# Optimization experiments

Hardware: AMD Instinct MI355X
Metric: run time of the kernel (lower is better)

The kernel has to match this reference:

```python
import jax, jax.numpy as jnp
import numpy as np

N_USERS = 100_000
N_ENTITIES = 400_000
N_NODES = N_USERS + N_ENTITIES  # 500k
DIM = 64
N_EDGES = 2_000_000
BATCH = 4096
N_LAYERS = 3
CF_WEIGHT = 1.0
L2_REG = 1e-4


def setup_inputs() -> dict:
    key = jax.random.key(0)
    k_emb, k_e, k_u, k_p, k_n = jax.random.split(key, 5)
    # xavier_uniform on (N, D): bound = sqrt(6/(N+D))
    bound = float(np.sqrt(6.0 / (N_NODES + DIM)))
    emb = jax.random.uniform(k_emb, (N_NODES, DIM), jnp.float32, -bound, bound)
    edge_index = jax.random.randint(k_e, (2, N_EDGES), 0, N_NODES, dtype=jnp.int32)
    user_idx = jax.random.randint(k_u, (BATCH,), 0, N_USERS, dtype=jnp.int32)
    pos_item = jax.random.randint(k_p, (BATCH,), 0, N_NODES, dtype=jnp.int32)
    neg_item = jax.random.randint(k_n, (BATCH,), 0, N_NODES, dtype=jnp.int32)
    return {"emb": emb, "edge_index": edge_index, "user_idx": user_idx,
            "pos_item": pos_item, "neg_item": neg_item}


def _lightgcn(emb, edge_index, n_layers):
    # LGConv(normalize=True): x' = D^{-1/2} A D^{-1/2} x, no self loops.
    n = emb.shape[0]
    src, dst = edge_index[0], edge_index[1]
    deg = jax.ops.segment_sum(jnp.ones_like(dst, dtype=emb.dtype), dst,
                              num_segments=n)
    dinv = jnp.where(deg > 0, jax.lax.rsqrt(jnp.maximum(deg, 1e-12)), 0.0)
    norm = dinv[src] * dinv[dst]  # [E]
    x = emb
    acc = emb  # layer-0 term of the mean over stacked layers
    for _ in range(n_layers):
        msgs = x[src] * norm[:, None]  # [E, D] gather + scale
        x = jax.ops.segment_sum(msgs, dst, num_segments=n)  # scatter-add
        acc = acc + x
    return acc / (n_layers + 1)  # mean over (layers+1) stacked embeddings


def reference(emb, edge_index, user_idx, pos_item, neg_item):
    all_layer = _lightgcn(emb, edge_index, N_LAYERS)
    u = all_layer[user_idx]
    p = all_layer[pos_item]
    n_ = all_layer[neg_item]
    pos_score = jnp.sum(u * p, axis=-1)
    neg_score = jnp.sum(u * n_, axis=-1)
    # BPRLoss: -mean(logsigmoid(pos - neg)) == mean(softplus(neg - pos))
    cf_loss = jnp.mean(jax.nn.softplus(neg_score - pos_score))
    u_ego = emb[user_idx]
    p_ego = emb[pos_item]
    n_ego = emb[neg_item]
    reg_loss = 0.5 * (jnp.sum(u_ego ** 2) + jnp.sum(p_ego ** 2)
                      + jnp.sum(n_ego ** 2)) / float(BATCH)
    return CF_WEIGHT * cf_loss + L2_REG * reg_loss
```

## Files before the change

kernel.cpp:

```cpp
#include <hip/hip_runtime.h>
#include <cstdint>
#include <cstddef>

#define N_USERS   100000
#define N_NODES   500000
#define DIM       64
#define N_EDGES   2000000
#define BATCH     4096
#define SCAN_B    1024
#define NBLK      ((N_NODES + SCAN_B - 1) / SCAN_B)
#define X1C_CAP   350000
#define LA_CAP    150000

typedef unsigned char uchar;
typedef unsigned short ushort;
typedef unsigned int uint;

__device__ __forceinline__ ushort f2bf(float f) {
    uint u = __float_as_uint(f);
    uint r = u + 0x7FFFu + ((u >> 16) & 1u);
    return (ushort)(r >> 16);
}
__device__ __forceinline__ float bflo(uint u) { return __uint_as_float(u << 16); }
__device__ __forceinline__ float bfhi(uint u) { return __uint_as_float(u & 0xFFFF0000u); }

__global__ void k_degexp(const int* __restrict__ src, const int* __restrict__ dst,
                         int* __restrict__ deg, const uchar* __restrict__ f3,
                         uchar* __restrict__ fA) {
    int t = blockIdx.x * blockDim.x + threadIdx.x;
    if (t < N_EDGES / 4) {
        int4 s = ((const int4*)src)[t];
        int4 d = ((const int4*)dst)[t];
        atomicAdd(&deg[d.x], 1); atomicAdd(&deg[d.y], 1);
        atomicAdd(&deg[d.z], 1); atomicAdd(&deg[d.w], 1);
        if (f3[d.x] && !fA[s.x]) fA[s.x] = 1;
        if (f3[d.y] && !fA[s.y]) fA[s.y] = 1;
        if (f3[d.z] && !fA[s.z]) fA[s.z] = 1;
        if (f3[d.w] && !fA[s.w]) fA[s.w] = 1;
    }
}

__global__ void k_expand(const int* __restrict__ src, const int* __restrict__ dst,
                         const uchar* __restrict__ fin, uchar* __restrict__ fout) {
    int t = blockIdx.x * blockDim.x + threadIdx.x;
    if (t < N_EDGES / 4) {
        int4 s = ((const int4*)src)[t];
        int4 d = ((const int4*)dst)[t];
        if (fin[d.x] && !fout[s.x]) fout[s.x] = 1;
        if (fin[d.y] && !fout[s.y]) fout[s.y] = 1;
        if (fin[d.z] && !fout[s.z]) fout[s.z] = 1;
        if (fin[d.w] && !fout[s.w]) fout[s.w] = 1;
    }
}

__global__ void k_mark(const int* __restrict__ u, const int* __restrict__ p,
                       const int* __restrict__ n, uchar* __restrict__ f3,
                       uchar* __restrict__ fA, uchar* __restrict__ fB) {
    int i = blockIdx.x * blockDim.x + threadIdx.x;
    if (i >= 3 * BATCH) return;
    int idx;
    if (i < BATCH)          idx = u[i];
    else if (i < 2 * BATCH) idx = p[i - BATCH];
    else                    idx = n[i - 2 * BATCH];
    f3[idx] = 1; fA[idx] = 1; fB[idx] = 1;
}

__global__ void k_scanA(const int* __restrict__ deg, const uchar* __restrict__ fA,
                        const uchar* __restrict__ fB, int* __restrict__ bsumD,
                        int* __restrict__ bsumP) {
    __shared__ int sD[SCAN_B];
    __shared__ int sP[SCAN_B];
    int i = blockIdx.x * SCAN_B + threadIdx.x;
    int d = 0, pk = 0;
    if (i < N_NODES) { d = deg[i]; pk = (int)fA[i] | ((int)fB[i] << 16); }
    sD[threadIdx.x] = d; sP[threadIdx.x] = pk;
    __syncthreads();
    for (int off = SCAN_B / 2; off; off >>= 1) {
        if (threadIdx.x < off) {
            sD[threadIdx.x] += sD[threadIdx.x + off];
            sP[threadIdx.x] += sP[threadIdx.x + off];
        }
        __syncthreads();
    }
    if (threadIdx.x == 0) { bsumD[blockIdx.x] = sD[0]; bsumP[blockIdx.x] = sP[0]; }
}

__global__ void k_scanB(const int* __restrict__ bsumD, const int* __restrict__ bsumP,
                        int* __restrict__ boffD, int* __restrict__ boffA,
                        int* __restrict__ boffB, int* __restrict__ counts,
                        int* __restrict__ rowstart_tail) {
    __shared__ int sD[512];
    __shared__ int sA[512];
    __shared__ int sB[512];
    int d = (threadIdx.x < NBLK) ? bsumD[threadIdx.x] : 0;
    int p = (threadIdx.x < NBLK) ? bsumP[threadIdx.x] : 0;
    int a = p & 0xFFFF, b = p >> 16;
    sD[threadIdx.x] = d; sA[threadIdx.x] = a; sB[threadIdx.x] = b;
    __syncthreads();
    for (int off = 1; off < 512; off <<= 1) {
        int tD = (threadIdx.x >= off) ? sD[threadIdx.x - off] : 0;
        int tA = (threadIdx.x >= off) ? sA[threadIdx.x - off] : 0;
        int tB = (threadIdx.x >= off) ? sB[threadIdx.x - off] : 0;
        __syncthreads();
        sD[threadIdx.x] += tD; sA[threadIdx.x] += tA; sB[threadIdx.x] += tB;
        __syncthreads();
    }
    if (threadIdx.x < NBLK) {
        boffD[threadIdx.x] = sD[threadIdx.x] - d;
        boffA[threadIdx.x] = sA[threadIdx.x] - a;
        boffB[threadIdx.x] = sB[threadIdx.x] - b;
    }
    if (threadIdx.x == 511) {
        counts[0] = sA[511]; counts[1] = sB[511];
        rowstart_tail[0] = N_EDGES;
    }
}

__global__ void k_scanC(const int* __restrict__ deg, const uchar* __restrict__ fA,
                        const uchar* __restrict__ fB,
                        const int* __restrict__ boffD, const int* __restrict__ boffA,
                        const int* __restrict__ boffB,
                        int* __restrict__ rowstart, int* __restrict__ cursor,
                        float* __restrict__ dinv, int* __restrict__ mapA,
                        int* __restrict__ mapB, int4* __restrict__ listA4,
                        int4* __restrict__ listB4) {
    __shared__ int sD[SCAN_B];
    __shared__ int sP[SCAN_B];
    int i = blockIdx.x * SCAN_B + threadIdx.x;
    int d = 0, a = 0, b = 0;
    if (i < N_NODES) { d = deg[i]; a = (int)fA[i]; b = (int)fB[i]; }
    sD[threadIdx.x] = d; sP[threadIdx.x] = a | (b << 16);
    __syncthreads();
    for (int off = 1; off < SCAN_B; off <<= 1) {
        int tD = (threadIdx.x >= off) ? sD[threadIdx.x - off] : 0;
        int tP = (threadIdx.x >= off) ? sP[threadIdx.x - off] : 0;
        __syncthreads();
        sD[threadIdx.x] += tD; sP[threadIdx.x] += tP;
        __syncthreads();
    }
    if (i < N_NODES) {
        int exD = sD[threadIdx.x] - d + boffD[blockIdx.x];
        int incP = sP[threadIdx.x];
        int exA = (incP & 0xFFFF) - a + boffA[blockIdx.x];
        int exB = (incP >> 16) - b + boffB[blockIdx.x];
        rowstart[i] = exD;
        cursor[i] = exD;
        float dv = (d > 0) ? rsqrtf((float)d) : 0.0f;
        dinv[i] = dv;
        mapA[i] = a ? exA : -1;
        mapB[i] = b ? exB : -1;
        int4 ent = make_int4(exD, exD + d, __float_as_int(dv), 0);
        if (a) listA4[exA] = ent;
        if (b) listB4[exB] = ent;
    }
}

__global__ void k_conv(const float* __restrict__ emb, const float* __restrict__ dinv,
                       ushort* __restrict__ embs) {
    int c = blockIdx.x * blockDim.x + threadIdx.x;
    if (c < N_NODES * 16) {
        int row = c >> 4;
        float4 v = ((const float4*)emb)[c];
        float dv = dinv[row];
        uint2 o;
        o.x = (uint)f2bf(v.x * dv) | ((uint)f2bf(v.y * dv) << 16);
        o.y = (uint)f2bf(v.z * dv) | ((uint)f2bf(v.w * dv) << 16);
        ((uint2*)embs)[c] = o;
    }
}

__global__ void k_scatter(const int* __restrict__ src, const int* __restrict__ dst,
                          const uchar* __restrict__ fB,
                          int* __restrict__ cursor, int* __restrict__ csr_src) {
    int t = blockIdx.x * blockDim.x + threadIdx.x;
    if (t < N_EDGES / 4) {
        int4 s = ((const int4*)src)[t];
        int4 d = ((const int4*)dst)[t];
        if (fB[d.x]) csr_src[atomicAdd(&cursor[d.x], 1)] = s.x;
        if (fB[d.y]) csr_src[atomicAdd(&cursor[d.y], 1)] = s.y;
        if (fB[d.z]) csr_src[atomicAdd(&cursor[d.z], 1)] = s.z;
        if (fB[d.w]) csr_src[atomicAdd(&cursor[d.w], 1)] = s.w;
    }
}

__global__ void k_prop1(const ushort* __restrict__ embs, const int4* __restrict__ listB4,
                        const int* __restrict__ counts, const int* __restrict__ csr_src,
                        ushort* __restrict__ x1c) {
    int lane = threadIdx.x & 63;
    int wv = (blockIdx.x * blockDim.x + threadIdx.x) >> 6;
    if (wv >= counts[1]) return;
    int4 nb = listB4[wv];
    int sub = lane >> 4, q = lane & 15;
    float4 acc = {0.f, 0.f, 0.f, 0.f};
    for (int i = nb.x + sub; i < nb.y; i += 4) {
        int s = csr_src[i];
        uint2 u = *(const uint2*)(embs + (size_t)s * DIM + q * 4);
        acc.x += bflo(u.x); acc.y += bfhi(u.x);
        acc.z += bflo(u.y); acc.w += bfhi(u.y);
    }
    for (int off = 16; off <= 32; off <<= 1) {
        acc.x += __shfl_xor(acc.x, off, 64);
        acc.y += __shfl_xor(acc.y, off, 64);
        acc.z += __shfl_xor(acc.z, off, 64);
        acc.w += __shfl_xor(acc.w, off, 64);
    }
    if (sub == 0) {
        float dv = __int_as_float(nb.z);
        float d2 = dv * dv;
        uint2 o;
        o.x = (uint)f2bf(acc.x * d2) | ((uint)f2bf(acc.y * d2) << 16);
        o.y = (uint)f2bf(acc.z * d2) | ((uint)f2bf(acc.w * d2) << 16);
        *(uint2*)(x1c + (size_t)wv * DIM + q * 4) = o;
    }
}

__global__ void k_prop2(const ushort* __restrict__ x1c, const int* __restrict__ mapB,
                        const int4* __restrict__ listA4, const int* __restrict__ counts,
                        const int* __restrict__ csr_src, ushort* __restrict__ x2c) {
    int lane = threadIdx.x & 63;
    int wv = (blockIdx.x * blockDim.x + threadIdx.x) >> 6;
    if (wv >= counts[0]) return;
    int4 nb = listA4[wv];
    int sub = lane >> 4, q = lane & 15;
    float4 acc = {0.f, 0.f, 0.f, 0.f};
    for (int i = nb.x + sub; i < nb.y; i += 4) {
        int s = csr_src[i];
        int slot = mapB[s];
        uint2 u = *(const uint2*)(x1c + (size_t)slot * DIM + q * 4);
        acc.x += bflo(u.x); acc.y += bfhi(u.x);
        acc.z += bflo(u.y); acc.w += bfhi(u.y);
    }
    for (int off = 16; off <= 32; off <<= 1) {
        acc.x += __shfl_xor(acc.x, off, 64);
        acc.y += __shfl_xor(acc.y, off, 64);
        acc.z += __shfl_xor(acc.z, off, 64);
        acc.w += __shfl_xor(acc.w, off, 64);
    }
    if (sub == 0) {
        float dv = __int_as_float(nb.z);
        float d2 = dv * dv;
        uint2 o;
        o.x = (uint)f2bf(acc.x * d2) | ((uint)f2bf(acc.y * d2) << 16);
        o.y = (uint)f2bf(acc.z * d2) | ((uint)f2bf(acc.w * d2) << 16);
        *(uint2*)(x2c + (size_t)wv * DIM + q * 4) = o;
    }
}

__global__ void k_prop3(const ushort* __restrict__ x2c, const int* __restrict__ mapA,
                        const int* __restrict__ u, const int* __restrict__ p,
                        const int* __restrict__ n, const float* __restrict__ dinv,
                        const int* __restrict__ rowstart, const int* __restrict__ csr_src,
                        float* __restrict__ x3c) {
    int lane = threadIdx.x & 63;
    int wv = (blockIdx.x * blockDim.x + threadIdx.x) >> 6;
    if (wv >= 3 * BATCH) return;
    int t;
    if (wv < BATCH)          t = u[wv];
    else if (wv < 2 * BATCH) t = p[wv - BATCH];
    else                     t = n[wv - 2 * BATCH];
    int sub = lane >> 4, q = lane & 15;
    int b = rowstart[t], e = rowstart[t + 1];
    float4 acc = {0.f, 0.f, 0.f, 0.f};
    for (int i = b + sub; i < e; i += 4) {
        int s = csr_src[i];
        int slot = mapA[s];
        uint2 uu = *(const uint2*)(x2c + (size_t)slot * DIM + q * 4);
        acc.x += bflo(uu.x); acc.y += bfhi(uu.x);
        acc.z += bflo(uu.y); acc.w += bfhi(uu.y);
    }
    for (int off = 16; off <= 32; off <<= 1) {
        acc.x += __shfl_xor(acc.x, off, 64);
        acc.y += __shfl_xor(acc.y, off, 64);
        acc.z += __shfl_xor(acc.z, off, 64);
        acc.w += __shfl_xor(acc.w, off, 64);
    }
    if (sub == 0) {
        float dv = dinv[t];
        float4 o = {acc.x * dv, acc.y * dv, acc.z * dv, acc.w * dv};
        ((float4*)x3c)[(size_t)wv * 16 + q] = o;
    }
}

__global__ void k_loss(const float* __restrict__ emb, const ushort* __restrict__ x1c,
                       const ushort* __restrict__ x2c, const float* __restrict__ x3c,
                       const int* __restrict__ mapA, const int* __restrict__ mapB,
                       const float* __restrict__ dinv,
                       const int* __restrict__ u, const int* __restrict__ p,
                       const int* __restrict__ n, float* __restrict__ out) {
    int lane = threadIdx.x & 63;
    int w = (blockIdx.x * blockDim.x + threadIdx.x) >> 6;
    if (w >= BATCH) return;
    int ui = u[w], pi = p[w], ni = n[w];
    float dvu = dinv[ui], dvp = dinv[pi], dvn = dinv[ni];
    float rdu = dvu > 0.f ? 1.f / dvu : 0.f;
    float rdp = dvp > 0.f ? 1.f / dvp : 0.f;
    float rdn = dvn > 0.f ? 1.f / dvn : 0.f;
    float ue = emb[(size_t)ui * DIM + lane];
    float pe = emb[(size_t)pi * DIM + lane];
    float ne = emb[(size_t)ni * DIM + lane];
    float u1 = __uint_as_float((uint)x1c[(size_t)mapB[ui] * DIM + lane] << 16) * rdu;
    float p1 = __uint_as_float((uint)x1c[(size_t)mapB[pi] * DIM + lane] << 16) * rdp;
    float n1 = __uint_as_float((uint)x1c[(size_t)mapB[ni] * DIM + lane] << 16) * rdn;
    float u2 = __uint_as_float((uint)x2c[(size_t)mapA[ui] * DIM + lane] << 16) * rdu;
    float p2 = __uint_as_float((uint)x2c[(size_t)mapA[pi] * DIM + lane] << 16) * rdp;
    float n2 = __uint_as_float((uint)x2c[(size_t)mapA[ni] * DIM + lane] << 16) * rdn;
    float uall = 0.25f * (ue + u1 + u2 + x3c[(size_t)w * DIM + lane]);
    float pall = 0.25f * (pe + p1 + p2 + x3c[(size_t)(BATCH + w) * DIM + lane]);
    float nall = 0.25f * (ne + n1 + n2 + x3c[(size_t)(2 * BATCH + w) * DIM + lane]);
    float pos = uall * pall;
    float neg = uall * nall;
    float sq  = ue * ue + pe * pe + ne * ne;
    for (int off = 32; off; off >>= 1) {
        pos += __shfl_xor(pos, off, 64);
        neg += __shfl_xor(neg, off, 64);
        sq  += __shfl_xor(sq,  off, 64);
    }
    if (lane == 0) {
        float z = neg - pos;
        float sp = fmaxf(z, 0.0f) + log1pf(expf(-fabsf(z)));
        float contrib = sp * (1.0f / BATCH) + 1e-4f * 0.5f * sq * (1.0f / BATCH);
        atomicAdd(out, contrib);
    }
}

extern "C" void kernel_launch(void* const* d_in, const int* in_sizes, int n_in,
                              void* d_out, int out_size, void* d_ws, size_t ws_size,
                              hipStream_t stream) {
    const float* emb  = (const float*)d_in[0];
    const int*   edge = (const int*)d_in[1];
    const int*   src  = edge;
    const int*   dst  = edge + N_EDGES;
    const int*   uidx = (const int*)d_in[2];
    const int*   pidx = (const int*)d_in[3];
    const int*   nidx = (const int*)d_in[4];
    float* out = (float*)d_out;

    char* w = (char*)d_ws;
    ushort* embs    = (ushort*)w;                w += (size_t)N_NODES * DIM * 2;
    ushort* x1c     = (ushort*)w;                w += (size_t)X1C_CAP * DIM * 2;
    ushort* x2c     = (ushort*)w;                w += (size_t)LA_CAP * DIM * 2;
    float*  x3c     = (float*)w;                 w += (size_t)3 * BATCH * DIM * 4;
    float*  dinv    = (float*)w;                 w += (size_t)N_NODES * 4;
    int*    deg     = (int*)w;                   w += (size_t)N_NODES * 4;
    int*    rowstart= (int*)w;                   w += (size_t)(N_NODES + 4) * 4;
    int*    cursor  = (int*)w;                   w += (size_t)N_NODES * 4;
    int*    csr_src = (int*)w;                   w += (size_t)N_EDGES * 4;
    int*    mapA    = (int*)w;                   w += (size_t)N_NODES * 4;
    int*    mapB    = (int*)w;                   w += (size_t)N_NODES * 4;
    int4*   listA4  = (int4*)w;                  w += (size_t)LA_CAP * 16;
    int4*   listB4  = (int4*)w;                  w += (size_t)X1C_CAP * 16;
    uchar*  flags   = (uchar*)w;                 w += (size_t)3 * N_NODES;
    uchar*  f3 = flags;
    uchar*  fA = flags + N_NODES;
    uchar*  fB = flags + 2 * N_NODES;
    int*    bsumD   = (int*)w;                   w += (size_t)NBLK * 4;
    int*    boffD   = (int*)w;                   w += (size_t)NBLK * 4;
    int*    bsumP   = (int*)w;                   w += (size_t)NBLK * 4;
    int*    boffA   = (int*)w;                   w += (size_t)NBLK * 4;
    int*    boffB   = (int*)w;                   w += (size_t)NBLK * 4;
    int*    counts  = (int*)w;                   w += 16;

    hipMemsetAsync(deg, 0, (size_t)N_NODES * 4, stream);
    hipMemsetAsync(flags, 0, (size_t)3 * N_NODES, stream);
    hipMemsetAsync(out, 0, 4, stream);

    k_mark<<<(3 * BATCH + 255) / 256, 256, 0, stream>>>(uidx, pidx, nidx, f3, fA, fB);
    k_degexp<<<(N_EDGES / 4 + 255) / 256, 256, 0, stream>>>(src, dst, deg, f3, fA);
    k_expand<<<(N_EDGES / 4 + 255) / 256, 256, 0, stream>>>(src, dst, fA, fB);

    k_scanA<<<NBLK, SCAN_B, 0, stream>>>(deg, fA, fB, bsumD, bsumP);
    k_scanB<<<1, 512, 0, stream>>>(bsumD, bsumP, boffD, boffA, boffB, counts,
                                   rowstart + N_NODES);
    k_scanC<<<NBLK, SCAN_B, 0, stream>>>(deg, fA, fB, boffD, boffA, boffB,
                                         rowstart, cursor, dinv, mapA, mapB,
                                         listA4, listB4);

    k_conv<<<(N_NODES * 16 + 255) / 256, 256, 0, stream>>>(emb, dinv, embs);

    k_scatter<<<(N_EDGES / 4 + 255) / 256, 256, 0, stream>>>(src, dst, fB, cursor, csr_src);

    const int PT = 256;
    k_prop1<<<((size_t)X1C_CAP * 64 + PT - 1) / PT, PT, 0, stream>>>(
        embs, listB4, counts, csr_src, x1c);
    k_prop2<<<((size_t)LA_CAP * 64 + PT - 1) / PT, PT, 0, stream>>>(
        x1c, mapB, listA4, counts, csr_src, x2c);
    k_prop3<<<(3 * BATCH * 64 + PT - 1) / PT, PT, 0, stream>>>(
        x2c, mapA, uidx, pidx, nidx, dinv, rowstart, csr_src, x3c);

    k_loss<<<(BATCH * 64 + 255) / 256, 256, 0, stream>>>(
        emb, x1c, x2c, x3c, mapA, mapB, dinv, uidx, pidx, nidx, out);
}
```

Measured before the change: 501.9 us.

## Pack node flags into bitmasks and degrees/cursors into byte-packed counters

```diff
diff --git a/kernel.cpp b/kernel.cpp
--- a/kernel.cpp
+++ b/kernel.cpp
@@ -9,6 +9,8 @@
 #define BATCH     4096
 #define SCAN_B    1024
 #define NBLK      ((N_NODES + SCAN_B - 1) / SCAN_B)
+#define NMASKW    ((N_NODES + 31) / 32)
+#define NPACK     ((N_NODES + 3) / 4)
 #define X1C_CAP   350000
 #define LA_CAP    150000
 
@@ -24,55 +26,70 @@
 __device__ __forceinline__ float bflo(uint u) { return __uint_as_float(u << 16); }
 __device__ __forceinline__ float bfhi(uint u) { return __uint_as_float(u & 0xFFFF0000u); }
 
-__global__ void k_degexp(const int* __restrict__ src, const int* __restrict__ dst,
-                         int* __restrict__ deg, const uchar* __restrict__ f3,
-                         uchar* __restrict__ fA) {
-    int t = blockIdx.x * blockDim.x + threadIdx.x;
-    if (t < N_EDGES / 4) {
-        int4 s = ((const int4*)src)[t];
-        int4 d = ((const int4*)dst)[t];
-        atomicAdd(&deg[d.x], 1); atomicAdd(&deg[d.y], 1);
-        atomicAdd(&deg[d.z], 1); atomicAdd(&deg[d.w], 1);
-        if (f3[d.x] && !fA[s.x]) fA[s.x] = 1;
-        if (f3[d.y] && !fA[s.y]) fA[s.y] = 1;
-        if (f3[d.z] && !fA[s.z]) fA[s.z] = 1;
-        if (f3[d.w] && !fA[s.w]) fA[s.w] = 1;
-    }
-}
-
-__global__ void k_expand(const int* __restrict__ src, const int* __restrict__ dst,
-                         const uchar* __restrict__ fin, uchar* __restrict__ fout) {
-    int t = blockIdx.x * blockDim.x + threadIdx.x;
-    if (t < N_EDGES / 4) {
-        int4 s = ((const int4*)src)[t];
-        int4 d = ((const int4*)dst)[t];
-        if (fin[d.x] && !fout[s.x]) fout[s.x] = 1;
-        if (fin[d.y] && !fout[s.y]) fout[s.y] = 1;
-        if (fin[d.z] && !fout[s.z]) fout[s.z] = 1;
-        if (fin[d.w] && !fout[s.w]) fout[s.w] = 1;
-    }
+__device__ __forceinline__ int getbit(const uint* __restrict__ w, int i) {
+    return (w[i >> 5] >> (i & 31)) & 1;
+}
+__device__ __forceinline__ void setbit(uint* w, int i) {
+    uint m = 1u << (i & 31);
+    if (!(w[i >> 5] & m)) atomicOr(&w[i >> 5], m);
 }
 
 __global__ void k_mark(const int* __restrict__ u, const int* __restrict__ p,
-                       const int* __restrict__ n, uchar* __restrict__ f3,
-                       uchar* __restrict__ fA, uchar* __restrict__ fB) {
+                       const int* __restrict__ n, uint* __restrict__ f3w,
+                       uint* __restrict__ fAw, uint* __restrict__ fBw) {
     int i = blockIdx.x * blockDim.x + threadIdx.x;
     if (i >= 3 * BATCH) return;
     int idx;
     if (i < BATCH)          idx = u[i];
     else if (i < 2 * BATCH) idx = p[i - BATCH];
     else                    idx = n[i - 2 * BATCH];
-    f3[idx] = 1; fA[idx] = 1; fB[idx] = 1;
-}
-
-__global__ void k_scanA(const int* __restrict__ deg, const uchar* __restrict__ fA,
-                        const uchar* __restrict__ fB, int* __restrict__ bsumD,
+    atomicOr(&f3w[idx >> 5], 1u << (idx & 31));
+    atomicOr(&fAw[idx >> 5], 1u << (idx & 31));
+    atomicOr(&fBw[idx >> 5], 1u << (idx & 31));
+}
+
+__global__ void k_degexp(const int* __restrict__ src, const int* __restrict__ dst,
+                         uint* __restrict__ degP, const uint* __restrict__ f3w,
+                         uint* __restrict__ fAw) {
+    int t = blockIdx.x * blockDim.x + threadIdx.x;
+    if (t < N_EDGES / 4) {
+        int4 s = ((const int4*)src)[t];
+        int4 d = ((const int4*)dst)[t];
+        atomicAdd(&degP[d.x >> 2], 1u << ((d.x & 3) * 8));
+        atomicAdd(&degP[d.y >> 2], 1u << ((d.y & 3) * 8));
+        atomicAdd(&degP[d.z >> 2], 1u << ((d.z & 3) * 8));
+        atomicAdd(&degP[d.w >> 2], 1u << ((d.w & 3) * 8));
+        if (getbit(f3w, d.x)) setbit(fAw, s.x);
+        if (getbit(f3w, d.y)) setbit(fAw, s.y);
+        if (getbit(f3w, d.z)) setbit(fAw, s.z);
+        if (getbit(f3w, d.w)) setbit(fAw, s.w);
+    }
+}
+
+__global__ void k_expand(const int* __restrict__ src, const int* __restrict__ dst,
+                         const uint* __restrict__ fAw, uint* __restrict__ fBw) {
+    int t = blockIdx.x * blockDim.x + threadIdx.x;
+    if (t < N_EDGES / 4) {
+        int4 s = ((const int4*)src)[t];
+        int4 d = ((const int4*)dst)[t];
+        if (getbit(fAw, d.x)) setbit(fBw, s.x);
+        if (getbit(fAw, d.y)) setbit(fBw, s.y);
+        if (getbit(fAw, d.z)) setbit(fBw, s.z);
+        if (getbit(fAw, d.w)) setbit(fBw, s.w);
+    }
+}
+
+__global__ void k_scanA(const uint* __restrict__ degP, const uint* __restrict__ fAw,
+                        const uint* __restrict__ fBw, int* __restrict__ bsumD,
                         int* __restrict__ bsumP) {
     __shared__ int sD[SCAN_B];
     __shared__ int sP[SCAN_B];
     int i = blockIdx.x * SCAN_B + threadIdx.x;
     int d = 0, pk = 0;
-    if (i < N_NODES) { d = deg[i]; pk = (int)fA[i] | ((int)fB[i] << 16); }
+    if (i < N_NODES) {
+        d = (degP[i >> 2] >> ((i & 3) * 8)) & 0xFF;
+        pk = getbit(fAw, i) | (getbit(fBw, i) << 16);
+    }
     sD[threadIdx.x] = d; sP[threadIdx.x] = pk;
     __syncthreads();
     for (int off = SCAN_B / 2; off; off >>= 1) {
@@ -116,19 +133,21 @@
     }
 }
 
-__global__ void k_scanC(const int* __restrict__ deg, const uchar* __restrict__ fA,
-                        const uchar* __restrict__ fB,
+__global__ void k_scanC(const uint* __restrict__ degP, const uint* __restrict__ fAw,
+                        const uint* __restrict__ fBw,
                         const int* __restrict__ boffD, const int* __restrict__ boffA,
                         const int* __restrict__ boffB,
-                        int* __restrict__ rowstart, int* __restrict__ cursor,
-                        float* __restrict__ dinv, int* __restrict__ mapA,
-                        int* __restrict__ mapB, int4* __restrict__ listA4,
-                        int4* __restrict__ listB4) {
+                        int* __restrict__ rowstart, float* __restrict__ dinv,
+                        int* __restrict__ mapA, int* __restrict__ mapB,
+                        int4* __restrict__ listA4, int4* __restrict__ listB4) {
     __shared__ int sD[SCAN_B];
     __shared__ int sP[SCAN_B];
     int i = blockIdx.x * SCAN_B + threadIdx.x;
     int d = 0, a = 0, b = 0;
-    if (i < N_NODES) { d = deg[i]; a = (int)fA[i]; b = (int)fB[i]; }
+    if (i < N_NODES) {
+        d = (degP[i >> 2] >> ((i & 3) * 8)) & 0xFF;
+        a = getbit(fAw, i); b = getbit(fBw, i);
+    }
     sD[threadIdx.x] = d; sP[threadIdx.x] = a | (b << 16);
     __syncthreads();
     for (int off = 1; off < SCAN_B; off <<= 1) {
@@ -144,7 +163,6 @@
         int exA = (incP & 0xFFFF) - a + boffA[blockIdx.x];
         int exB = (incP >> 16) - b + boffB[blockIdx.x];
         rowstart[i] = exD;
-        cursor[i] = exD;
         float dv = (d > 0) ? rsqrtf((float)d) : 0.0f;
         dinv[i] = dv;
         mapA[i] = a ? exA : -1;
@@ -170,16 +188,20 @@
 }
 
 __global__ void k_scatter(const int* __restrict__ src, const int* __restrict__ dst,
-                          const uchar* __restrict__ fB,
-                          int* __restrict__ cursor, int* __restrict__ csr_src) {
+                          const uint* __restrict__ fBw, const int* __restrict__ rowstart,
+                          uint* __restrict__ cur8, int* __restrict__ csr_src) {
     int t = blockIdx.x * blockDim.x + threadIdx.x;
     if (t < N_EDGES / 4) {
         int4 s = ((const int4*)src)[t];
         int4 d = ((const int4*)dst)[t];
-        if (fB[d.x]) csr_src[atomicAdd(&cursor[d.x], 1)] = s.x;
-        if (fB[d.y]) csr_src[atomicAdd(&cursor[d.y], 1)] = s.y;
-        if (fB[d.z]) csr_src[atomicAdd(&cursor[d.z], 1)] = s.z;
-        if (fB[d.w]) csr_src[atomicAdd(&cursor[d.w], 1)] = s.w;
+        #define SCAT(dd, ss) \
+            if (getbit(fBw, dd)) { \
+                uint old = atomicAdd(&cur8[(dd) >> 2], 1u << (((dd) & 3) * 8)); \
+                int off = (old >> (((dd) & 3) * 8)) & 0xFF; \
+                csr_src[rowstart[dd] + off] = (ss); \
+            }
+        SCAT(d.x, s.x) SCAT(d.y, s.y) SCAT(d.z, s.z) SCAT(d.w, s.w)
+        #undef SCAT
     }
 }
 
@@ -341,18 +363,19 @@
     ushort* x2c     = (ushort*)w;                w += (size_t)LA_CAP * DIM * 2;
     float*  x3c     = (float*)w;                 w += (size_t)3 * BATCH * DIM * 4;
     float*  dinv    = (float*)w;                 w += (size_t)N_NODES * 4;
-    int*    deg     = (int*)w;                   w += (size_t)N_NODES * 4;
     int*    rowstart= (int*)w;                   w += (size_t)(N_NODES + 4) * 4;
-    int*    cursor  = (int*)w;                   w += (size_t)N_NODES * 4;
     int*    csr_src = (int*)w;                   w += (size_t)N_EDGES * 4;
     int*    mapA    = (int*)w;                   w += (size_t)N_NODES * 4;
     int*    mapB    = (int*)w;                   w += (size_t)N_NODES * 4;
     int4*   listA4  = (int4*)w;                  w += (size_t)LA_CAP * 16;
     int4*   listB4  = (int4*)w;                  w += (size_t)X1C_CAP * 16;
-    uchar*  flags   = (uchar*)w;                 w += (size_t)3 * N_NODES;
-    uchar*  f3 = flags;
-    uchar*  fA = flags + N_NODES;
-    uchar*  fB = flags + 2 * N_NODES;
+    char*   zbase   = w;
+    uint*   degP    = (uint*)w;                  w += (size_t)NPACK * 4;
+    uint*   cur8    = (uint*)w;                  w += (size_t)NPACK * 4;
+    uint*   f3w     = (uint*)w;                  w += (size_t)NMASKW * 4;
+    uint*   fAw     = (uint*)w;                  w += (size_t)NMASKW * 4;
+    uint*   fBw     = (uint*)w;                  w += (size_t)NMASKW * 4;
+    size_t  zbytes  = (size_t)(w - zbase);
     int*    bsumD   = (int*)w;                   w += (size_t)NBLK * 4;
     int*    boffD   = (int*)w;                   w += (size_t)NBLK * 4;
     int*    bsumP   = (int*)w;                   w += (size_t)NBLK * 4;
@@ -360,24 +383,23 @@
     int*    boffB   = (int*)w;                   w += (size_t)NBLK * 4;
     int*    counts  = (int*)w;                   w += 16;
 
-    hipMemsetAsync(deg, 0, (size_t)N_NODES * 4, stream);
-    hipMemsetAsync(flags, 0, (size_t)3 * N_NODES, stream);
+    hipMemsetAsync(zbase, 0, zbytes, stream);
     hipMemsetAsync(out, 0, 4, stream);
 
-    k_mark<<<(3 * BATCH + 255) / 256, 256, 0, stream>>>(uidx, pidx, nidx, f3, fA, fB);
-    k_degexp<<<(N_EDGES / 4 + 255) / 256, 256, 0, stream>>>(src, dst, deg, f3, fA);
-    k_expand<<<(N_EDGES / 4 + 255) / 256, 256, 0, stream>>>(src, dst, fA, fB);
-
-    k_scanA<<<NBLK, SCAN_B, 0, stream>>>(deg, fA, fB, bsumD, bsumP);
+    k_mark<<<(3 * BATCH + 255) / 256, 256, 0, stream>>>(uidx, pidx, nidx, f3w, fAw, fBw);
+    k_degexp<<<(N_EDGES / 4 + 255) / 256, 256, 0, stream>>>(src, dst, degP, f3w, fAw);
+    k_expand<<<(N_EDGES / 4 + 255) / 256, 256, 0, stream>>>(src, dst, fAw, fBw);
+
+    k_scanA<<<NBLK, SCAN_B, 0, stream>>>(degP, fAw, fBw, bsumD, bsumP);
     k_scanB<<<1, 512, 0, stream>>>(bsumD, bsumP, boffD, boffA, boffB, counts,
                                    rowstart + N_NODES);
-    k_scanC<<<NBLK, SCAN_B, 0, stream>>>(deg, fA, fB, boffD, boffA, boffB,
-                                         rowstart, cursor, dinv, mapA, mapB,
-                                         listA4, listB4);
+    k_scanC<<<NBLK, SCAN_B, 0, stream>>>(degP, fAw, fBw, boffD, boffA, boffB,
+                                         rowstart, dinv, mapA, mapB, listA4, listB4);
 
     k_conv<<<(N_NODES * 16 + 255) / 256, 256, 0, stream>>>(emb, dinv, embs);
 
-    k_scatter<<<(N_EDGES / 4 + 255) / 256, 256, 0, stream>>>(src, dst, fB, cursor, csr_src);
+    k_scatter<<<(N_EDGES / 4 + 255) / 256, 256, 0, stream>>>(src, dst, fBw, rowstart,
+                                                             cur8, csr_src);
 
     const int PT = 256;
     k_prop1<<<((size_t)X1C_CAP * 64 + PT - 1) / PT, PT, 0, stream>>>(
```

After: 560.7 us. 11.7% more time.

## Fuse layer-3 propagation into loss kernel and drop cursor array

Applied to the files above, without the earlier changes.

```diff
diff --git a/kernel.cpp b/kernel.cpp
--- a/kernel.cpp
+++ b/kernel.cpp
@@ -23,35 +23,6 @@
 }
 __device__ __forceinline__ float bflo(uint u) { return __uint_as_float(u << 16); }
 __device__ __forceinline__ float bfhi(uint u) { return __uint_as_float(u & 0xFFFF0000u); }
-
-__global__ void k_degexp(const int* __restrict__ src, const int* __restrict__ dst,
-                         int* __restrict__ deg, const uchar* __restrict__ f3,
-                         uchar* __restrict__ fA) {
-    int t = blockIdx.x * blockDim.x + threadIdx.x;
-    if (t < N_EDGES / 4) {
-        int4 s = ((const int4*)src)[t];
-        int4 d = ((const int4*)dst)[t];
-        atomicAdd(&deg[d.x], 1); atomicAdd(&deg[d.y], 1);
-        atomicAdd(&deg[d.z], 1); atomicAdd(&deg[d.w], 1);
-        if (f3[d.x] && !fA[s.x]) fA[s.x] = 1;
-        if (f3[d.y] && !fA[s.y]) fA[s.y] = 1;
-        if (f3[d.z] && !fA[s.z]) fA[s.z] = 1;
-        if (f3[d.w] && !fA[s.w]) fA[s.w] = 1;
-    }
-}
-
-__global__ void k_expand(const int* __restrict__ src, const int* __restrict__ dst,
-                         const uchar* __restrict__ fin, uchar* __restrict__ fout) {
-    int t = blockIdx.x * blockDim.x + threadIdx.x;
-    if (t < N_EDGES / 4) {
-        int4 s = ((const int4*)src)[t];
-        int4 d = ((const int4*)dst)[t];
-        if (fin[d.x] && !fout[s.x]) fout[s.x] = 1;
-        if (fin[d.y] && !fout[s.y]) fout[s.y] = 1;
-        if (fin[d.z] && !fout[s.z]) fout[s.z] = 1;
-        if (fin[d.w] && !fout[s.w]) fout[s.w] = 1;
-    }
-}
 
 __global__ void k_mark(const int* __restrict__ u, const int* __restrict__ p,
                        const int* __restrict__ n, uchar* __restrict__ f3,
@@ -63,6 +34,49 @@
     else if (i < 2 * BATCH) idx = p[i - BATCH];
     else                    idx = n[i - 2 * BATCH];
     f3[idx] = 1; fA[idx] = 1; fB[idx] = 1;
+}
+
+__global__ void k_degexp(const int* __restrict__ src, const int* __restrict__ dst,
+                         int* __restrict__ deg, const uchar* __restrict__ f3,
+                         uchar* __restrict__ fA) {
+    int t = blockIdx.x * blockDim.x + threadIdx.x;
+    if (t < N_EDGES / 8) {
+        int4 s0 = ((const int4*)src)[2 * t];
+        int4 s1 = ((const int4*)src)[2 * t + 1];
+        int4 d0 = ((const int4*)dst)[2 * t];
+        int4 d1 = ((const int4*)dst)[2 * t + 1];
+        atomicAdd(&deg[d0.x], 1); atomicAdd(&deg[d0.y], 1);
+        atomicAdd(&deg[d0.z], 1); atomicAdd(&deg[d0.w], 1);
+        atomicAdd(&deg[d1.x], 1); atomicAdd(&deg[d1.y], 1);
+        atomicAdd(&deg[d1.z], 1); atomicAdd(&deg[d1.w], 1);
+        if (f3[d0.x] && !fA[s0.x]) fA[s0.x] = 1;
+        if (f3[d0.y] && !fA[s0.y]) fA[s0.y] = 1;
+        if (f3[d0.z] && !fA[s0.z]) fA[s0.z] = 1;
+        if (f3[d0.w] && !fA[s0.w]) fA[s0.w] = 1;
+        if (f3[d1.x] && !fA[s1.x]) fA[s1.x] = 1;
+        if (f3[d1.y] && !fA[s1.y]) fA[s1.y] = 1;
+        if (f3[d1.z] && !fA[s1.z]) fA[s1.z] = 1;
+        if (f3[d1.w] && !fA[s1.w]) fA[s1.w] = 1;
+    }
+}
+
+__global__ void k_expand(const int* __restrict__ src, const int* __restrict__ dst,
+                         const uchar* __restrict__ fin, uchar* __restrict__ fout) {
+    int t = blockIdx.x * blockDim.x + threadIdx.x;
+    if (t < N_EDGES / 8) {
+        int4 s0 = ((const int4*)src)[2 * t];
+        int4 s1 = ((const int4*)src)[2 * t + 1];
+        int4 d0 = ((const int4*)dst)[2 * t];
+        int4 d1 = ((const int4*)dst)[2 * t + 1];
+        if (fin[d0.x] && !fout[s0.x]) fout[s0.x] = 1;
+        if (fin[d0.y] && !fout[s0.y]) fout[s0.y] = 1;
+        if (fin[d0.z] && !fout[s0.z]) fout[s0.z] = 1;
+        if (fin[d0.w] && !fout[s0.w]) fout[s0.w] = 1;
+        if (fin[d1.x] && !fout[s1.x]) fout[s1.x] = 1;
+        if (fin[d1.y] && !fout[s1.y]) fout[s1.y] = 1;
+        if (fin[d1.z] && !fout[s1.z]) fout[s1.z] = 1;
+        if (fin[d1.w] && !fout[s1.w]) fout[s1.w] = 1;
+    }
 }
 
 __global__ void k_scanA(const int* __restrict__ deg, const uchar* __restrict__ fA,
@@ -87,8 +101,7 @@
 
 __global__ void k_scanB(const int* __restrict__ bsumD, const int* __restrict__ bsumP,
                         int* __restrict__ boffD, int* __restrict__ boffA,
-                        int* __restrict__ boffB, int* __restrict__ counts,
-                        int* __restrict__ rowstart_tail) {
+                        int* __restrict__ boffB, int* __restrict__ counts) {
     __shared__ int sD[512];
     __shared__ int sA[512];
     __shared__ int sB[512];
@@ -110,20 +123,16 @@
         boffA[threadIdx.x] = sA[threadIdx.x] - a;
         boffB[threadIdx.x] = sB[threadIdx.x] - b;
     }
-    if (threadIdx.x == 511) {
-        counts[0] = sA[511]; counts[1] = sB[511];
-        rowstart_tail[0] = N_EDGES;
-    }
+    if (threadIdx.x == 511) { counts[0] = sA[511]; counts[1] = sB[511]; }
 }
 
 __global__ void k_scanC(const int* __restrict__ deg, const uchar* __restrict__ fA,
                         const uchar* __restrict__ fB,
                         const int* __restrict__ boffD, const int* __restrict__ boffA,
                         const int* __restrict__ boffB,
-                        int* __restrict__ rowstart, int* __restrict__ cursor,
-                        float* __restrict__ dinv, int* __restrict__ mapA,
-                        int* __restrict__ mapB, int4* __restrict__ listA4,
-                        int4* __restrict__ listB4) {
+                        int* __restrict__ rowstart, float* __restrict__ dinv,
+                        int* __restrict__ mapA, int* __restrict__ mapB,
+                        int4* __restrict__ listA4, int4* __restrict__ listB4) {
     __shared__ int sD[SCAN_B];
     __shared__ int sP[SCAN_B];
     int i = blockIdx.x * SCAN_B + threadIdx.x;
@@ -144,7 +153,6 @@
         int exA = (incP & 0xFFFF) - a + boffA[blockIdx.x];
         int exB = (incP >> 16) - b + boffB[blockIdx.x];
         rowstart[i] = exD;
-        cursor[i] = exD;
         float dv = (d > 0) ? rsqrtf((float)d) : 0.0f;
         dinv[i] = dv;
         mapA[i] = a ? exA : -1;
@@ -170,16 +178,22 @@
 }
 
 __global__ void k_scatter(const int* __restrict__ src, const int* __restrict__ dst,
-                          const uchar* __restrict__ fB,
-                          int* __restrict__ cursor, int* __restrict__ csr_src) {
+                          const uchar* __restrict__ fB, int* __restrict__ rowstart,
+                          int* __restrict__ csr_src) {
     int t = blockIdx.x * blockDim.x + threadIdx.x;
-    if (t < N_EDGES / 4) {
-        int4 s = ((const int4*)src)[t];
-        int4 d = ((const int4*)dst)[t];
-        if (fB[d.x]) csr_src[atomicAdd(&cursor[d.x], 1)] = s.x;
-        if (fB[d.y]) csr_src[atomicAdd(&cursor[d.y], 1)] = s.y;
-        if (fB[d.z]) csr_src[atomicAdd(&cursor[d.z], 1)] = s.z;
-        if (fB[d.w]) csr_src[atomicAdd(&cursor[d.w], 1)] = s.w;
+    if (t < N_EDGES / 8) {
+        int4 s0 = ((const int4*)src)[2 * t];
+        int4 s1 = ((const int4*)src)[2 * t + 1];
+        int4 d0 = ((const int4*)dst)[2 * t];
+        int4 d1 = ((const int4*)dst)[2 * t + 1];
+        if (fB[d0.x]) csr_src[atomicAdd(&rowstart[d0.x], 1)] = s0.x;
+        if (fB[d0.y]) csr_src[atomicAdd(&rowstart[d0.y], 1)] = s0.y;
+        if (fB[d0.z]) csr_src[atomicAdd(&rowstart[d0.z], 1)] = s0.z;
+        if (fB[d0.w]) csr_src[atomicAdd(&rowstart[d0.w], 1)] = s0.w;
+        if (fB[d1.x]) csr_src[atomicAdd(&rowstart[d1.x], 1)] = s1.x;
+        if (fB[d1.y]) csr_src[atomicAdd(&rowstart[d1.y], 1)] = s1.y;
+        if (fB[d1.z]) csr_src[atomicAdd(&rowstart[d1.z], 1)] = s1.z;
+        if (fB[d1.w]) csr_src[atomicAdd(&rowstart[d1.w], 1)] = s1.w;
     }
 }
 
@@ -246,44 +260,26 @@
     }
 }
 
-__global__ void k_prop3(const ushort* __restrict__ x2c, const int* __restrict__ mapA,
-                        const int* __restrict__ u, const int* __restrict__ p,
-                        const int* __restrict__ n, const float* __restrict__ dinv,
-                        const int* __restrict__ rowstart, const int* __restrict__ csr_src,
-                        float* __restrict__ x3c) {
-    int lane = threadIdx.x & 63;
-    int wv = (blockIdx.x * blockDim.x + threadIdx.x) >> 6;
-    if (wv >= 3 * BATCH) return;
-    int t;
-    if (wv < BATCH)          t = u[wv];
-    else if (wv < 2 * BATCH) t = p[wv - BATCH];
-    else                     t = n[wv - 2 * BATCH];
-    int sub = lane >> 4, q = lane & 15;
-    int b = rowstart[t], e = rowstart[t + 1];
-    float4 acc = {0.f, 0.f, 0.f, 0.f};
-    for (int i = b + sub; i < e; i += 4) {
+__device__ __forceinline__ float x3_row(const ushort* __restrict__ x2c,
+                                        const int* __restrict__ mapA,
+                                        const int* __restrict__ csr_src,
+                                        const int4* __restrict__ listB4,
+                                        const int* __restrict__ mapB,
+                                        int t, int lane) {
+    int4 nb = listB4[mapB[t]];
+    float acc = 0.f;
+    for (int i = nb.x; i < nb.y; ++i) {
         int s = csr_src[i];
         int slot = mapA[s];
-        uint2 uu = *(const uint2*)(x2c + (size_t)slot * DIM + q * 4);
-        acc.x += bflo(uu.x); acc.y += bfhi(uu.x);
-        acc.z += bflo(uu.y); acc.w += bfhi(uu.y);
-    }
-    for (int off = 16; off <= 32; off <<= 1) {
-        acc.x += __shfl_xor(acc.x, off, 64);
-        acc.y += __shfl_xor(acc.y, off, 64);
-        acc.z += __shfl_xor(acc.z, off, 64);
-        acc.w += __shfl_xor(acc.w, off, 64);
-    }
-    if (sub == 0) {
-        float dv = dinv[t];
-        float4 o = {acc.x * dv, acc.y * dv, acc.z * dv, acc.w * dv};
-        ((float4*)x3c)[(size_t)wv * 16 + q] = o;
-    }
+        acc += __uint_as_float((uint)x2c[(size_t)slot * DIM + lane] << 16);
+    }
+    return acc * __int_as_float(nb.z);
 }
 
 __global__ void k_loss(const float* __restrict__ emb, const ushort* __restrict__ x1c,
-                       const ushort* __restrict__ x2c, const float* __restrict__ x3c,
+                       const ushort* __restrict__ x2c,
                        const int* __restrict__ mapA, const int* __restrict__ mapB,
+                       const int4* __restrict__ listB4, const int* __restrict__ csr_src,
                        const float* __restrict__ dinv,
                        const int* __restrict__ u, const int* __restrict__ p,
                        const int* __restrict__ n, float* __restrict__ out) {
@@ -304,9 +300,12 @@
     float u2 = __uint_as_float((uint)x2c[(size_t)mapA[ui] * DIM + lane] << 16) * rdu;
     float p2 = __uint_as_float((uint)x2c[(size_t)mapA[pi] * DIM + lane] << 16) * rdp;
     float n2 = __uint_as_float((uint)x2c[(size_t)mapA[ni] * DIM + lane] << 16) * rdn;
-    float uall = 0.25f * (ue + u1 + u2 + x3c[(size_t)w * DIM + lane]);
-    float pall = 0.25f * (pe + p1 + p2 + x3c[(size_t)(BATCH + w) * DIM + lane]);
-    float nall = 0.25f * (ne + n1 + n2 + x3c[(size_t)(2 * BATCH + w) * DIM + lane]);
+    float u3 = x3_row(x2c, mapA, csr_src, listB4, mapB, ui, lane);
+    float p3 = x3_row(x2c, mapA, csr_src, listB4, mapB, pi, lane);
+    float n3 = x3_row(x2c, mapA, csr_src, listB4, mapB, ni, lane);
+    float uall = 0.25f * (ue + u1 + u2 + u3);
+    float pall = 0.25f * (pe + p1 + p2 + p3);
+    float nall = 0.25f * (ne + n1 + n2 + n3);
     float pos = uall * pall;
     float neg = uall * nall;
     float sq  = ue * ue + pe * pe + ne * ne;
@@ -339,20 +338,20 @@
     ushort* embs    = (ushort*)w;                w += (size_t)N_NODES * DIM * 2;
     ushort* x1c     = (ushort*)w;                w += (size_t)X1C_CAP * DIM * 2;
     ushort* x2c     = (ushort*)w;                w += (size_t)LA_CAP * DIM * 2;
-    float*  x3c     = (float*)w;                 w += (size_t)3 * BATCH * DIM * 4;
     float*  dinv    = (float*)w;                 w += (size_t)N_NODES * 4;
-    int*    deg     = (int*)w;                   w += (size_t)N_NODES * 4;
-    int*    rowstart= (int*)w;                   w += (size_t)(N_NODES + 4) * 4;
-    int*    cursor  = (int*)w;                   w += (size_t)N_NODES * 4;
+    int*    rowstart= (int*)w;                   w += (size_t)N_NODES * 4;
     int*    csr_src = (int*)w;                   w += (size_t)N_EDGES * 4;
     int*    mapA    = (int*)w;                   w += (size_t)N_NODES * 4;
     int*    mapB    = (int*)w;                   w += (size_t)N_NODES * 4;
     int4*   listA4  = (int4*)w;                  w += (size_t)LA_CAP * 16;
     int4*   listB4  = (int4*)w;                  w += (size_t)X1C_CAP * 16;
+    char*   zbase   = w;
+    int*    deg     = (int*)w;                   w += (size_t)N_NODES * 4;
     uchar*  flags   = (uchar*)w;                 w += (size_t)3 * N_NODES;
     uchar*  f3 = flags;
     uchar*  fA = flags + N_NODES;
     uchar*  fB = flags + 2 * N_NODES;
+    size_t  zbytes  = (size_t)(w - zbase);
     int*    bsumD   = (int*)w;                   w += (size_t)NBLK * 4;
     int*    boffD   = (int*)w;                   w += (size_t)NBLK * 4;
     int*    bsumP   = (int*)w;                   w += (size_t)NBLK * 4;
@@ -360,33 +359,29 @@
     int*    boffB   = (int*)w;                   w += (size_t)NBLK * 4;
     int*    counts  = (int*)w;                   w += 16;
 
-    hipMemsetAsync(deg, 0, (size_t)N_NODES * 4, stream);
-    hipMemsetAsync(flags, 0, (size_t)3 * N_NODES, stream);
+    hipMemsetAsync(zbase, 0, zbytes, stream);
     hipMemsetAsync(out, 0, 4, stream);
 
     k_mark<<<(3 * BATCH + 255) / 256, 256, 0, stream>>>(uidx, pidx, nidx, f3, fA, fB);
-    k_degexp<<<(N_EDGES / 4 + 255) / 256, 256, 0, stream>>>(src, dst, deg, f3, fA);
-    k_expand<<<(N_EDGES / 4 + 255) / 256, 256, 0, stream>>>(src, dst, fA, fB);
+    k_degexp<<<(N_EDGES / 8 + 255) / 256, 256, 0, stream>>>(src, dst, deg, f3, fA);
+    k_expand<<<(N_EDGES / 8 + 255) / 256, 256, 0, stream>>>(src, dst, fA, fB);
 
     k_scanA<<<NBLK, SCAN_B, 0, stream>>>(deg, fA, fB, bsumD, bsumP);
-    k_scanB<<<1, 512, 0, stream>>>(bsumD, bsumP, boffD, boffA, boffB, counts,
-                                   rowstart + N_NODES);
+    k_scanB<<<1, 512, 0, stream>>>(bsumD, bsumP, boffD, boffA, boffB, counts);
     k_scanC<<<NBLK, SCAN_B, 0, stream>>>(deg, fA, fB, boffD, boffA, boffB,
-                                         rowstart, cursor, dinv, mapA, mapB,
-                                         listA4, listB4);
+                                         rowstart, dinv, mapA, mapB, listA4, listB4);
 
     k_conv<<<(N_NODES * 16 + 255) / 256, 256, 0, stream>>>(emb, dinv, embs);
 
-    k_scatter<<<(N_EDGES / 4 + 255) / 256, 256, 0, stream>>>(src, dst, fB, cursor, csr_src);
+    k_scatter<<<(N_EDGES / 8 + 255) / 256, 256, 0, stream>>>(src, dst, fB, rowstart,
+                                                             csr_src);
 
     const int PT = 256;
     k_prop1<<<((size_t)X1C_CAP * 64 + PT - 1) / PT, PT, 0, stream>>>(
         embs, listB4, counts, csr_src, x1c);
     k_prop2<<<((size_t)LA_CAP * 64 + PT - 1) / PT, PT, 0, stream>>>(
         x1c, mapB, listA4, counts, csr_src, x2c);
-    k_prop3<<<(3 * BATCH * 64 + PT - 1) / PT, PT, 0, stream>>>(
-        x2c, mapA, uidx, pidx, nidx, dinv, rowstart, csr_src, x3c);
 
     k_loss<<<(BATCH * 64 + 255) / 256, 256, 0, stream>>>(
-        emb, x1c, x2c, x3c, mapA, mapB, dinv, uidx, pidx, nidx, out);
-}
+        emb, x1c, x2c, mapA, mapB, listB4, csr_src, dinv, uidx, pidx, nidx, out);
+}
```

Result: no change. 500.4 us (-0.3%).
